# Performance work log

Measured on AMD Instinct MI355X. Metric: run time of the kernel, lower is better.

Reference implementation:

```python
import jax, jax.numpy as jnp
import numpy as np

EMBED_DIM = 1024
HEADS = 16
D_HEAD = EMBED_DIM // HEADS
B, S = 2, 2048


def setup_inputs() -> dict:
    key = jax.random.key(0)
    ks = jax.random.split(key, 7)
    scale = 1.0 / np.sqrt(EMBED_DIM)
    inp = {
        "key": jax.random.normal(ks[0], (B, S, EMBED_DIM), dtype=jnp.float32),
        "query": jax.random.normal(ks[1], (B, S, EMBED_DIM), dtype=jnp.float32),
        "value": jax.random.normal(ks[2], (B, S, EMBED_DIM), dtype=jnp.float32),
        # causal mask, broadcastable to [B, H, Sq, Sk]
        "mask": jnp.tril(jnp.ones((S, S), dtype=bool))[None, None, :, :],
        # torch nn.Linear weights: [out_features, in_features], applied as x @ W.T
        "Wq": jax.random.normal(ks[3], (EMBED_DIM, EMBED_DIM), dtype=jnp.float32) * scale,
        "Wk": jax.random.normal(ks[4], (EMBED_DIM, EMBED_DIM), dtype=jnp.float32) * scale,
        "Wv": jax.random.normal(ks[5], (EMBED_DIM, EMBED_DIM), dtype=jnp.float32) * scale,
        "Wo": jax.random.normal(ks[6], (EMBED_DIM, EMBED_DIM), dtype=jnp.float32) * scale,
    }
    return inp


def reference(key, query, value, mask, Wq, Wk, Wv, Wo):
    b, sq, _ = query.shape
    sk = key.shape[1]
    # projections (torch Linear: x @ W.T), reshape to [B, H, S, Dh]
    q = (query @ Wq.T).reshape(b, sq, HEADS, D_HEAD).transpose(0, 2, 1, 3)
    k = (key @ Wk.T).reshape(b, sk, HEADS, D_HEAD).transpose(0, 2, 1, 3)
    v = (value @ Wv.T).reshape(b, sk, HEADS, D_HEAD).transpose(0, 2, 1, 3)
    # scaled dot-product scores [B, H, Sq, Sk]
    scores = jnp.einsum("bhqd,bhkd->bhqk", q, k) / jnp.sqrt(jnp.float32(D_HEAD))
    scores = jnp.where(mask, scores, jnp.float32(-1e9))
    attn = jax.nn.softmax(scores, axis=-1)
    # dropout p=0.0 -> identity
    out = jnp.einsum("bhqk,bhkd->bhqd", attn, v)  # [B, H, Sq, Dh]
    out = out.transpose(0, 2, 1, 3).reshape(b, sq, EMBED_DIM)
    return out @ Wo.T
```

## Files before the change

kernel.cpp:

```cpp
#include <hip/hip_runtime.h>
#include <stdint.h>


typedef unsigned short ushort_t;
typedef __attribute__((ext_vector_type(8))) __bf16 bf16x8;
typedef __attribute__((ext_vector_type(4))) float floatx4;

#define EMBED 1024
#define SEQ   2048
#define NH    16
#define DH    64
#define QK_SCALE 0.18033688011112042f

__device__ inline ushort_t f2b(float x) {
  unsigned u = __float_as_uint(x);
  u += 0x7FFFu + ((u >> 16) & 1u);
  return (ushort_t)(u >> 16);
}

__device__ inline unsigned pk2(float a, float b) {
  unsigned ua = __float_as_uint(a) + 0x8000u;
  unsigned ub = __float_as_uint(b) + 0x8000u;
  return __builtin_amdgcn_perm(ub, ua, 0x07060302u);
}

__device__ inline void gl_lds16(const ushort_t* g, ushort_t* l) {
  __builtin_amdgcn_global_load_lds(
      (const __attribute__((address_space(1))) unsigned int*)g,
      (__attribute__((address_space(3))) unsigned int*)l, 16, 0, 0);
}

struct CvtArgs {
  const float* src[16];
  ushort_t*    dst[16];
  float        scale[16];
};

__global__ __launch_bounds__(256) void cvt_kernel(CvtArgs a) {
  const int chunk = blockIdx.x >> 9;
  const int off = ((blockIdx.x & 511) << 11) + (threadIdx.x << 3);
  const float sc = a.scale[chunk];
  const float4* s = (const float4*)(a.src[chunk] + off);
  float4 f0 = s[0], f1 = s[1];
  union { ushort_t u[8]; uint4 v; } o;
  o.u[0] = f2b(f0.x * sc); o.u[1] = f2b(f0.y * sc);
  o.u[2] = f2b(f0.z * sc); o.u[3] = f2b(f0.w * sc);
  o.u[4] = f2b(f1.x * sc); o.u[5] = f2b(f1.y * sc);
  o.u[6] = f2b(f1.z * sc); o.u[7] = f2b(f1.w * sc);
  *(uint4*)(a.dst[chunk] + off) = o.v;
}

__device__ inline void store_sub(char* __restrict__ Cv, const int mode,
                                 const int ldc, const int row, const int col,
                                 const floatx4& acc) {
  if (mode == 0) {
    ushort_t* C = (ushort_t*)Cv;
#pragma unroll
    for (int r = 0; r < 4; ++r)
      C[(size_t)(row + r) * ldc + col] = f2b(acc[r]);
  } else if (mode == 1) {
    float* C = (float*)Cv;
#pragma unroll
    for (int r = 0; r < 4; ++r)
      C[(size_t)(row + r) * ldc + col] = acc[r];
  } else {
    ushort_t* C = (ushort_t*)Cv;
    const int b = row >> 11, s = row & 2047;
    const int h = col >> 6, d = col & 63;
    uint2 pk;
    pk.x = pk2(acc[0], acc[1]);
    pk.y = pk2(acc[2], acc[3]);
    *(uint2*)&C[(size_t)((b * NH + h) * DH + d) * SEQ + s] = pk;
  }
}

__device__ inline void gemm512_core(const ushort_t* __restrict__ A,
                                    const ushort_t* __restrict__ W,
                                    char* __restrict__ Cv, const int mode,
                                    const int ldc, const int m0, const int n0) {
  __shared__ ushort_t As[32 * 512];
  __shared__ ushort_t Bs[16 * 512];
  const int tid  = threadIdx.x;
  const int lane = tid & 63;
  const int wid  = tid >> 6;
  const int lm   = lane & 15;
  const int quad = lane >> 4;
  const int wm   = wid >> 1;
  const int wn   = wid & 1;

  floatx4 zero = {0.f, 0.f, 0.f, 0.f};
  floatx4 acc[4][4];
#pragma unroll
  for (int i = 0; i < 4; ++i)
#pragma unroll
    for (int j = 0; j < 4; ++j) acc[i][j] = zero;

  for (int k0 = 0; k0 < EMBED; k0 += 64) {
    __syncthreads();
#pragma unroll
    for (int u = 0; u < 6; ++u) {
      const int c   = wid * 6 + u;
      const int cb  = c & 31;
      const int sub = cb >> 1;
      const int kc  = (cb & 1) * 32 + quad * 8;
      if (c < 32)
        gl_lds16(A + (size_t)(m0 + sub * 16 + lm) * EMBED + k0 + kc, &As[cb * 512]);
      else
        gl_lds16(W + (size_t)(n0 + sub * 16 + lm) * EMBED + k0 + kc, &Bs[cb * 512]);
    }
    __syncthreads();

#pragma unroll
    for (int ks = 0; ks < 2; ++ks) {
      bf16x8 a[4], b[4];
#pragma unroll
      for (int i = 0; i < 4; ++i)
        a[i] = *(const bf16x8*)&As[((wm * 4 + i) * 2 + ks) * 512 + lane * 8];
#pragma unroll
      for (int j = 0; j < 4; ++j)
        b[j] = *(const bf16x8*)&Bs[((wn * 4 + j) * 2 + ks) * 512 + lane * 8];
#pragma unroll
      for (int i = 0; i < 4; ++i)
#pragma unroll
        for (int j = 0; j < 4; ++j)
          acc[i][j] = __builtin_amdgcn_mfma_f32_16x16x32_bf16(a[i], b[j], acc[i][j], 0, 0, 0);
    }
  }

#pragma unroll
  for (int i = 0; i < 4; ++i) {
    const int row = m0 + wm * 64 + i * 16 + quad * 4;
#pragma unroll
    for (int j = 0; j < 4; ++j)
      store_sub(Cv, mode, ldc, row, n0 + wn * 64 + j * 16 + lm, acc[i][j]);
  }
}

struct QkvArgs {
  const ushort_t* A[3];
  const ushort_t* W[3];
  char*           C[3];
};

__global__ __launch_bounds__(512, 4) void qkv_gemm(QkvArgs q) {
  const int z = blockIdx.z;
  gemm512_core(q.A[z], q.W[z], q.C[z], z == 2 ? 2 : 0, EMBED,
               blockIdx.x * 256, blockIdx.y * 128);
}

__global__ __launch_bounds__(256) void o_gemm(const ushort_t* __restrict__ A,
                                              const ushort_t* __restrict__ W,
                                              float* __restrict__ C) {
  __shared__ ushort_t As[16 * 512];
  __shared__ ushort_t Bs[16 * 512];
  const int m0 = blockIdx.x * 128, n0 = blockIdx.y * 128;
  const int tid  = threadIdx.x;
  const int lane = tid & 63;
  const int wid  = tid >> 6;
  const int lm   = lane & 15;
  const int quad = lane >> 4;

  floatx4 zero = {0.f, 0.f, 0.f, 0.f};
  floatx4 acc[4][4];
#pragma unroll
  for (int i = 0; i < 4; ++i)
#pragma unroll
    for (int j = 0; j < 4; ++j) acc[i][j] = zero;

  const int tm = (wid >> 1) * 4;
  const int tn = (wid & 1) * 4;

  for (int k0 = 0; k0 < EMBED; k0 += 64) {
    __syncthreads();
#pragma unroll
    for (int u = 0; u < 8; ++u) {
      const int c   = wid * 8 + u;
      const int cb  = c & 15;
      const int sub = cb >> 1;
      const int kc  = (cb & 1) * 32 + quad * 8;
      if (c < 16)
        gl_lds16(A + (size_t)(m0 + sub * 16 + lm) * EMBED + k0 + kc, &As[cb * 512]);
      else
        gl_lds16(W + (size_t)(n0 + sub * 16 + lm) * EMBED + k0 + kc, &Bs[cb * 512]);
    }
    __syncthreads();

#pragma unroll
    for (int ks = 0; ks < 2; ++ks) {
      bf16x8 a[4], b[4];
#pragma unroll
      for (int i = 0; i < 4; ++i)
        a[i] = *(const bf16x8*)&As[((tm + i) * 2 + ks) * 512 + lane * 8];
#pragma unroll
      for (int j = 0; j < 4; ++j)
        b[j] = *(const bf16x8*)&Bs[((tn + j) * 2 + ks) * 512 + lane * 8];
#pragma unroll
      for (int i = 0; i < 4; ++i)
#pragma unroll
        for (int j = 0; j < 4; ++j)
          acc[i][j] = __builtin_amdgcn_mfma_f32_16x16x32_bf16(a[i], b[j], acc[i][j], 0, 0, 0);
    }
  }

#pragma unroll
  for (int i = 0; i < 4; ++i) {
    const int row = m0 + (wid >> 1) * 64 + i * 16 + quad * 4;
#pragma unroll
    for (int j = 0; j < 4; ++j) {
      const int col = n0 + (wid & 1) * 64 + j * 16 + lm;
#pragma unroll
      for (int r = 0; r < 4; ++r)
        C[(size_t)(row + r) * EMBED + col] = acc[i][j][r];
    }
  }
}

__global__ __launch_bounds__(256) void attn_kernel(const ushort_t* __restrict__ Qp,
                                                   const ushort_t* __restrict__ Kp,
                                                   const ushort_t* __restrict__ VpT,
                                                   ushort_t* __restrict__ Ob) {
  __shared__ ushort_t Qs[16 * 512];
  __shared__ ushort_t Ks[2][8 * 512];
  __shared__ ushort_t VTs[2][8 * 512];
  __shared__ ushort_t Pw[4 * 2048];
  const int L = blockIdx.x;
  const int qb = (L < 256) ? (15 - (L >> 5)) : ((L >> 5) - 8);
  const int bh = L & 31;
  const int h = bh & (NH - 1), b = bh >> 4;
  const int tid = threadIdx.x, lane = tid & 63, wid = tid >> 6;
  const int lm = lane & 15, quad = lane >> 4;
  const size_t qkbase = ((size_t)b * SEQ) * EMBED + h * DH;
  const size_t vtbase = ((size_t)(b * NH + h)) * DH * SEQ;
  ushort_t* pwb = &Pw[wid * 2048];

#pragma unroll
  for (int u = 0; u < 4; ++u) {
    const int c = wid * 4 + u;
    gl_lds16(Qp + qkbase + (size_t)(qb * 128 + (c >> 1) * 16 + lm) * EMBED
                 + (c & 1) * 32 + quad * 8,
             &Qs[c * 512]);
  }
#pragma unroll
  for (int u = 0; u < 4; ++u) {
    const int t = wid * 4 + u;
    const int cb = t & 7, sub = cb >> 1, half = cb & 1;
    if (t < 8)
      gl_lds16(Kp + qkbase + (size_t)(sub * 16 + lm) * EMBED + half * 32 + quad * 8,
               &Ks[0][cb * 512]);
    else
      gl_lds16(VpT + vtbase + (size_t)(sub * 16 + lm) * SEQ + half * 32 + quad * 8,
               &VTs[0][cb * 512]);
  }
  asm volatile("s_waitcnt vmcnt(4)" ::: "memory");
  bf16x8 qf[2][2];
#pragma unroll
  for (int qg = 0; qg < 2; ++qg)
#pragma unroll
    for (int ks = 0; ks < 2; ++ks)
      qf[qg][ks] = *(const bf16x8*)&Qs[((wid * 2 + qg) * 2 + ks) * 512 + lane * 8];

  float l_part[2] = {0.f, 0.f};
  floatx4 zero = {0.f, 0.f, 0.f, 0.f};
  floatx4 o_acc[4][2];
#pragma unroll
  for (int d = 0; d < 4; ++d)
#pragma unroll
    for (int qg = 0; qg < 2; ++qg) o_acc[d][qg] = zero;

  const int kt_end = 2 * qb + 1;
  for (int kt = 0; kt <= kt_end; ++kt) {
    const int cur = kt & 1;
    asm volatile("s_waitcnt vmcnt(0)" ::: "memory");
    __syncthreads();
    if (kt < kt_end) {
      const int kn = kt + 1;
#pragma unroll
      for (int u = 0; u < 4; ++u) {
        const int t = wid * 4 + u;
        const int cb = t & 7, sub = cb >> 1, half = cb & 1;
        if (t < 8)
          gl_lds16(Kp + qkbase + (size_t)(kn * 64 + sub * 16 + lm) * EMBED
                       + half * 32 + quad * 8,
                   &Ks[cur ^ 1][cb * 512]);
        else
          gl_lds16(VpT + vtbase + (size_t)(sub * 16 + lm) * SEQ
                       + kn * 64 + half * 32 + quad * 8,
                   &VTs[cur ^ 1][cb * 512]);
      }
    }

    floatx4 s_acc[4][2];
#pragma unroll
    for (int i = 0; i < 4; ++i)
#pragma unroll
      for (int qg = 0; qg < 2; ++qg) s_acc[i][qg] = zero;
#pragma unroll
    for (int ks = 0; ks < 2; ++ks)
#pragma unroll
      for (int i = 0; i < 4; ++i) {
        bf16x8 kf = *(const bf16x8*)&Ks[cur][(i * 2 + ks) * 512 + lane * 8];
#pragma unroll
        for (int qg = 0; qg < 2; ++qg)
          s_acc[i][qg] = __builtin_amdgcn_mfma_f32_16x16x32_bf16(kf, qf[qg][ks], s_acc[i][qg], 0, 0, 0);
      }

    const bool diag = (kt >= 2 * qb);
#pragma unroll
    for (int i = 0; i < 4; ++i) {
      const int s = i >> 1;
      const int quadB = ((i & 1) << 1) | (quad >> 1);
      const int gkk = kt * 64 + i * 16 + quad * 4;
#pragma unroll
      for (int qg = 0; qg < 2; ++qg) {
        float p[4];
#pragma unroll
        for (int r = 0; r < 4; ++r) p[r] = __builtin_amdgcn_exp2f(s_acc[i][qg][r]);
        if (diag) {
          const int gq = qb * 128 + wid * 32 + qg * 16 + lm;
#pragma unroll
          for (int r = 0; r < 4; ++r)
            if (gkk + r > gq) p[r] = 0.f;
        }
#pragma unroll
        for (int r = 0; r < 4; ++r) l_part[qg] += p[r];
        uint2 pk;
        pk.x = pk2(p[0], p[1]);
        pk.y = pk2(p[2], p[3]);
        *(uint2*)&pwb[(qg * 2 + s) * 512 + (quadB * 16 + lm) * 8 + ((quad & 1) << 2)] = pk;
      }
    }
    asm volatile("s_waitcnt lgkmcnt(0)" ::: "memory");

#pragma unroll
    for (int s = 0; s < 2; ++s) {
      bf16x8 pf[2];
#pragma unroll
      for (int qg = 0; qg < 2; ++qg)
        pf[qg] = *(const bf16x8*)&pwb[(qg * 2 + s) * 512 + lane * 8];
#pragma unroll
      for (int d = 0; d < 4; ++d) {
        bf16x8 vf = *(const bf16x8*)&VTs[cur][(d * 2 + s) * 512 + lane * 8];
#pragma unroll
        for (int qg = 0; qg < 2; ++qg)
          o_acc[d][qg] = __builtin_amdgcn_mfma_f32_16x16x32_bf16(vf, pf[qg], o_acc[d][qg], 0, 0, 0);
      }
    }
  }

#pragma unroll
  for (int qg = 0; qg < 2; ++qg) {
    float l = l_part[qg];
    l += __shfl_xor(l, 16, 64);
    l += __shfl_xor(l, 32, 64);
    const float inv_l = 1.0f / l;
    const size_t orow = qkbase + (size_t)(qb * 128 + wid * 32 + qg * 16 + lm) * EMBED;
#pragma unroll
    for (int d = 0; d < 4; ++d) {
      uint2 pk;
      pk.x = pk2(o_acc[d][qg][0] * inv_l, o_acc[d][qg][1] * inv_l);
      pk.y = pk2(o_acc[d][qg][2] * inv_l, o_acc[d][qg][3] * inv_l);
      *(uint2*)&Ob[orow + d * 16 + quad * 4] = pk;
    }
  }
}

extern "C" void kernel_launch(void* const* d_in, const int* in_sizes, int n_in,
                              void* d_out, int out_size, void* d_ws, size_t ws_size,
                              hipStream_t stream) {
  const float* key   = (const float*)d_in[0];
  const float* query = (const float*)d_in[1];
  const float* value = (const float*)d_in[2];
  const float* Wq = (const float*)d_in[4];
  const float* Wk = (const float*)d_in[5];
  const float* Wv = (const float*)d_in[6];
  const float* Wo = (const float*)d_in[7];

  char* ws = (char*)d_ws;
  const size_t MB = 1024 * 1024;
  ushort_t* Xk  = (ushort_t*)(ws + 0 * MB);
  ushort_t* Xq  = (ushort_t*)(ws + 8 * MB);
  ushort_t* Xv  = (ushort_t*)(ws + 16 * MB);
  ushort_t* Wqb = (ushort_t*)(ws + 24 * MB);
  ushort_t* Wkb = (ushort_t*)(ws + 26 * MB);
  ushort_t* Wvb = (ushort_t*)(ws + 28 * MB);
  ushort_t* Wob = (ushort_t*)(ws + 30 * MB);
  ushort_t* Qp  = (ushort_t*)(ws + 32 * MB);
  ushort_t* Kp  = (ushort_t*)(ws + 40 * MB);
  ushort_t* VpT = (ushort_t*)(ws + 48 * MB);
  ushort_t* Ob  = (ushort_t*)(ws + 56 * MB);

  CvtArgs ca;
  const size_t CE = 1048576;
  for (int c = 0; c < 16; ++c) ca.scale[c] = 1.0f;
  for (int c = 0; c < 4; ++c) { ca.src[c]     = key   + c * CE; ca.dst[c]     = Xk + c * CE; }
  for (int c = 0; c < 4; ++c) { ca.src[4 + c] = query + c * CE; ca.dst[4 + c] = Xq + c * CE; }
  for (int c = 0; c < 4; ++c) { ca.src[8 + c] = value + c * CE; ca.dst[8 + c] = Xv + c * CE; }
  ca.src[12] = Wq; ca.dst[12] = Wqb; ca.scale[12] = QK_SCALE;
  ca.src[13] = Wk; ca.dst[13] = Wkb;
  ca.src[14] = Wv; ca.dst[14] = Wvb;
  ca.src[15] = Wo; ca.dst[15] = Wob;
  cvt_kernel<<<8192, 256, 0, stream>>>(ca);

  QkvArgs qa;
  qa.A[0] = Xq; qa.W[0] = Wqb; qa.C[0] = (char*)Qp;
  qa.A[1] = Xk; qa.W[1] = Wkb; qa.C[1] = (char*)Kp;
  qa.A[2] = Xv; qa.W[2] = Wvb; qa.C[2] = (char*)VpT;
  qkv_gemm<<<dim3(16, 8, 3), 512, 0, stream>>>(qa);

  attn_kernel<<<512, 256, 0, stream>>>(Qp, Kp, VpT, Ob);

  o_gemm<<<dim3(32, 8), 256, 0, stream>>>(Ob, Wob, (float*)d_out);
}
```

Measured before the change: 253.3 us.

## Halve attention query tile to 64 rows and double block count

The attention kernel now processes 64 query rows per block instead of 128, so each wave owns 16 query rows and the grid doubles to 1024 blocks. The P staging buffer reuses the Q shared-memory region, which cuts LDS use and, with launch_bounds(256,4), is meant to allow more resident blocks per CU. Block-to-tile mapping is rearranged to interleave short and long causal tiles for load balance. In exchange, K/V tiles are reloaded by twice as many blocks and each wave does less MFMA work per K/V load.

Result: faster. 244.1 us (-3.6%).

```diff
diff --git a/kernel.cpp b/kernel.cpp
--- a/kernel.cpp
+++ b/kernel.cpp
@@ -215,28 +215,31 @@
   }
 }
 
-__global__ __launch_bounds__(256) void attn_kernel(const ushort_t* __restrict__ Qp,
-                                                   const ushort_t* __restrict__ Kp,
-                                                   const ushort_t* __restrict__ VpT,
-                                                   ushort_t* __restrict__ Ob) {
-  __shared__ ushort_t Qs[16 * 512];
+__global__ __launch_bounds__(256, 4) void attn_kernel(const ushort_t* __restrict__ Qp,
+                                                      const ushort_t* __restrict__ Kp,
+                                                      const ushort_t* __restrict__ VpT,
+                                                      ushort_t* __restrict__ Ob) {
+  __shared__ ushort_t Qs[8 * 512];
   __shared__ ushort_t Ks[2][8 * 512];
   __shared__ ushort_t VTs[2][8 * 512];
-  __shared__ ushort_t Pw[4 * 2048];
   const int L = blockIdx.x;
-  const int qb = (L < 256) ? (15 - (L >> 5)) : ((L >> 5) - 8);
+  const int s8 = (L >> 5) & 7;
+  const int g  = L >> 8;
+  const int qb = (g == 0) ? s8
+               : (g == 1) ? (15 - s8)
+               : (g == 2) ? (16 + s8)
+                          : (31 - s8);
   const int bh = L & 31;
   const int h = bh & (NH - 1), b = bh >> 4;
   const int tid = threadIdx.x, lane = tid & 63, wid = tid >> 6;
   const int lm = lane & 15, quad = lane >> 4;
   const size_t qkbase = ((size_t)b * SEQ) * EMBED + h * DH;
   const size_t vtbase = ((size_t)(b * NH + h)) * DH * SEQ;
-  ushort_t* pwb = &Pw[wid * 2048];
-
-#pragma unroll
-  for (int u = 0; u < 4; ++u) {
-    const int c = wid * 4 + u;
-    gl_lds16(Qp + qkbase + (size_t)(qb * 128 + (c >> 1) * 16 + lm) * EMBED
+
+#pragma unroll
+  for (int u = 0; u < 2; ++u) {
+    const int c = wid * 2 + u;
+    gl_lds16(Qp + qkbase + (size_t)(qb * 64 + (c >> 1) * 16 + lm) * EMBED
                  + (c & 1) * 32 + quad * 8,
              &Qs[c * 512]);
   }
@@ -252,27 +255,23 @@
                &VTs[0][cb * 512]);
   }
   asm volatile("s_waitcnt vmcnt(4)" ::: "memory");
-  bf16x8 qf[2][2];
-#pragma unroll
-  for (int qg = 0; qg < 2; ++qg)
-#pragma unroll
-    for (int ks = 0; ks < 2; ++ks)
-      qf[qg][ks] = *(const bf16x8*)&Qs[((wid * 2 + qg) * 2 + ks) * 512 + lane * 8];
-
-  float l_part[2] = {0.f, 0.f};
+  bf16x8 qf[2];
+#pragma unroll
+  for (int ks = 0; ks < 2; ++ks)
+    qf[ks] = *(const bf16x8*)&Qs[(wid * 2 + ks) * 512 + lane * 8];
+  ushort_t* pwb = &Qs[wid * 1024];
+
+  float l_part = 0.f;
   floatx4 zero = {0.f, 0.f, 0.f, 0.f};
-  floatx4 o_acc[4][2];
-#pragma unroll
-  for (int d = 0; d < 4; ++d)
-#pragma unroll
-    for (int qg = 0; qg < 2; ++qg) o_acc[d][qg] = zero;
-
-  const int kt_end = 2 * qb + 1;
-  for (int kt = 0; kt <= kt_end; ++kt) {
+  floatx4 o_acc[4];
+#pragma unroll
+  for (int d = 0; d < 4; ++d) o_acc[d] = zero;
+
+  for (int kt = 0; kt <= qb; ++kt) {
     const int cur = kt & 1;
     asm volatile("s_waitcnt vmcnt(0)" ::: "memory");
     __syncthreads();
-    if (kt < kt_end) {
+    if (kt < qb) {
       const int kn = kt + 1;
 #pragma unroll
       for (int u = 0; u < 4; ++u) {
@@ -289,76 +288,63 @@
       }
     }
 
-    floatx4 s_acc[4][2];
-#pragma unroll
-    for (int i = 0; i < 4; ++i)
-#pragma unroll
-      for (int qg = 0; qg < 2; ++qg) s_acc[i][qg] = zero;
+    floatx4 s_acc[4];
+#pragma unroll
+    for (int i = 0; i < 4; ++i) s_acc[i] = zero;
 #pragma unroll
     for (int ks = 0; ks < 2; ++ks)
 #pragma unroll
       for (int i = 0; i < 4; ++i) {
         bf16x8 kf = *(const bf16x8*)&Ks[cur][(i * 2 + ks) * 512 + lane * 8];
-#pragma unroll
-        for (int qg = 0; qg < 2; ++qg)
-          s_acc[i][qg] = __builtin_amdgcn_mfma_f32_16x16x32_bf16(kf, qf[qg][ks], s_acc[i][qg], 0, 0, 0);
+        s_acc[i] = __builtin_amdgcn_mfma_f32_16x16x32_bf16(kf, qf[ks], s_acc[i], 0, 0, 0);
       }
 
-    const bool diag = (kt >= 2 * qb);
+    const bool diag = (kt == qb);
 #pragma unroll
     for (int i = 0; i < 4; ++i) {
-      const int s = i >> 1;
+      const int sH = i >> 1;
       const int quadB = ((i & 1) << 1) | (quad >> 1);
       const int gkk = kt * 64 + i * 16 + quad * 4;
-#pragma unroll
-      for (int qg = 0; qg < 2; ++qg) {
-        float p[4];
-#pragma unroll
-        for (int r = 0; r < 4; ++r) p[r] = __builtin_amdgcn_exp2f(s_acc[i][qg][r]);
-        if (diag) {
-          const int gq = qb * 128 + wid * 32 + qg * 16 + lm;
-#pragma unroll
-          for (int r = 0; r < 4; ++r)
-            if (gkk + r > gq) p[r] = 0.f;
-        }
-#pragma unroll
-        for (int r = 0; r < 4; ++r) l_part[qg] += p[r];
-        uint2 pk;
-        pk.x = pk2(p[0], p[1]);
-        pk.y = pk2(p[2], p[3]);
-        *(uint2*)&pwb[(qg * 2 + s) * 512 + (quadB * 16 + lm) * 8 + ((quad & 1) << 2)] = pk;
+      float p[4];
+#pragma unroll
+      for (int r = 0; r < 4; ++r) p[r] = __builtin_amdgcn_exp2f(s_acc[i][r]);
+      if (diag) {
+        const int gq = qb * 64 + wid * 16 + lm;
+#pragma unroll
+        for (int r = 0; r < 4; ++r)
+          if (gkk + r > gq) p[r] = 0.f;
       }
+#pragma unroll
+      for (int r = 0; r < 4; ++r) l_part += p[r];
+      uint2 pk;
+      pk.x = pk2(p[0], p[1]);
+      pk.y = pk2(p[2], p[3]);
+      *(uint2*)&pwb[sH * 512 + (quadB * 16 + lm) * 8 + ((quad & 1) << 2)] = pk;
     }
     asm volatile("s_waitcnt lgkmcnt(0)" ::: "memory");
 
 #pragma unroll
-    for (int s = 0; s < 2; ++s) {
-      bf16x8 pf[2];
-#pragma unroll
-      for (int qg = 0; qg < 2; ++qg)
-        pf[qg] = *(const bf16x8*)&pwb[(qg * 2 + s) * 512 + lane * 8];
+    for (int sH = 0; sH < 2; ++sH) {
+      bf16x8 pf = *(const bf16x8*)&pwb[sH * 512 + lane * 8];
 #pragma unroll
       for (int d = 0; d < 4; ++d) {
-        bf16x8 vf = *(const bf16x8*)&VTs[cur][(d * 2 + s) * 512 + lane * 8];
-#pragma unroll
-        for (int qg = 0; qg < 2; ++qg)
-          o_acc[d][qg] = __builtin_amdgcn_mfma_f32_16x16x32_bf16(vf, pf[qg], o_acc[d][qg], 0, 0, 0);
+        bf16x8 vf = *(const bf16x8*)&VTs[cur][(d * 2 + sH) * 512 + lane * 8];
+        o_acc[d] = __builtin_amdgcn_mfma_f32_16x16x32_bf16(vf, pf, o_acc[d], 0, 0, 0);
       }
     }
   }
 
-#pragma unroll
-  for (int qg = 0; qg < 2; ++qg) {
-    float l = l_part[qg];
+  {
+    float l = l_part;
     l += __shfl_xor(l, 16, 64);
     l += __shfl_xor(l, 32, 64);
     const float inv_l = 1.0f / l;
-    const size_t orow = qkbase + (size_t)(qb * 128 + wid * 32 + qg * 16 + lm) * EMBED;
+    const size_t orow = qkbase + (size_t)(qb * 64 + wid * 16 + lm) * EMBED;
 #pragma unroll
     for (int d = 0; d < 4; ++d) {
       uint2 pk;
-      pk.x = pk2(o_acc[d][qg][0] * inv_l, o_acc[d][qg][1] * inv_l);
-      pk.y = pk2(o_acc[d][qg][2] * inv_l, o_acc[d][qg][3] * inv_l);
+      pk.x = pk2(o_acc[d][0] * inv_l, o_acc[d][1] * inv_l);
+      pk.y = pk2(o_acc[d][2] * inv_l, o_acc[d][3] * inv_l);
       *(uint2*)&Ob[orow + d * 16 + quad * 4] = pk;
     }
   }
@@ -407,7 +393,7 @@
   qa.A[2] = Xv; qa.W[2] = Wvb; qa.C[2] = (char*)VpT;
   qkv_gemm<<<dim3(16, 8, 3), 512, 0, stream>>>(qa);
 
-  attn_kernel<<<512, 256, 0, stream>>>(Qp, Kp, VpT, Ob);
+  attn_kernel<<<1024, 256, 0, stream>>>(Qp, Kp, VpT, Ob);
 
   o_gemm<<<dim3(32, 8), 256, 0, stream>>>(Ob, Wob, (float*)d_out);
 }
```
